# Kernel tuning notes

Hardware: AMD Instinct MI355X
Metric: run time of the kernel (lower is better)

Reference implementation:

```python
import jax, jax.numpy as jnp
import numpy as np

N_SUPPORT = 12800
N_QUERY = 32768
SEQ_LEN = 100
INPUT_DIM = 32
EMBED_DIM = 64
N_CLASSES = 128
EPS = 1e-8


def setup_inputs() -> dict:
    key = jax.random.key(0)
    k1, k2, k3 = jax.random.split(key, 3)
    support = jax.random.normal(k1, (N_SUPPORT, SEQ_LEN, INPUT_DIM), dtype=jnp.float32)
    query = jax.random.normal(k2, (N_QUERY, SEQ_LEN, INPUT_DIM), dtype=jnp.float32)
    # equal shots per class; unique() first-occurrence order == 0..C-1
    support_labels = jnp.arange(N_SUPPORT, dtype=jnp.int64 if jax.config.jax_enable_x64 else jnp.int32) % N_CLASSES
    W = jax.random.normal(k3, (INPUT_DIM, EMBED_DIM), dtype=jnp.float32) * (1.0 / np.sqrt(INPUT_DIM))
    b = jnp.zeros((EMBED_DIM,), dtype=jnp.float32)
    return {"support": support, "support_labels": support_labels, "query": query, "W": W, "b": b}


def _encode(x, W, b):
    # minimal encoder: mean-pool over seq, then linear projection
    return jnp.mean(x, axis=1) @ W + b  # (n, embed_dim)


def reference(support, support_labels, query, W, b):
    se = _encode(support, W, b)   # (n_support, D)
    qe = _encode(query, W, b)     # (n_query, D)
    # per-class mean (segment mean), single fused pass instead of per-class boolean_mask loop
    sums = jax.ops.segment_sum(se, support_labels, num_segments=N_CLASSES)          # (C, D)
    counts = jax.ops.segment_sum(jnp.ones((se.shape[0],), se.dtype), support_labels, num_segments=N_CLASSES)
    prototypes = sums / counts[:, None]                                             # (C, D)
    # pairwise euclidean distance, faithful to expand-subtract-sum formulation
    diff = qe[:, None, :] - prototypes[None, :, :]                                  # (n_query, C, D)
    distances = jnp.sqrt(jnp.sum(diff * diff, axis=2) + EPS)                        # (n_query, C)
    logits = -jnp.square(distances)
    return logits, prototypes
```

## Files before the change

kernel.cpp:

```cpp
#include <hip/hip_runtime.h>

#define SEQ_LEN   100
#define IN_DIM    32
#define EMB       64
#define NCLS      128
#define N_SUPPORT 12800
#define N_QUERY   32768
#define N_ITEMS   (N_SUPPORT + N_QUERY)
#define EPS_F     1e-8f


__global__ __launch_bounds__(256) void zero_ws_k(float* __restrict__ ws, int n) {
    int i = blockIdx.x * 256 + threadIdx.x;
    if (i < n) ws[i] = 0.0f;
}

__global__ __launch_bounds__(256) void encode_all_k(
    const float* __restrict__ support, const int* __restrict__ labels,
    const float* __restrict__ query,   const float* __restrict__ W,
    const float* __restrict__ b,
    float* __restrict__ classSum, float* __restrict__ classCount,
    float* __restrict__ qe)
{
    __shared__ float Wl[IN_DIM * EMB];
    const int t = threadIdx.x;
    #pragma unroll
    for (int j = 0; j < 8; ++j) Wl[t + j * 256] = W[t + j * 256];

    const int lane = t & 63;
    const int wave = t >> 6;
    const int d4 = lane & 7;
    const int ph = lane >> 3;
    const float bd = b[lane];
    __syncthreads();

    const int nWaves = gridDim.x * 4;
    const float s = 1.0f / (float)SEQ_LEN;

    for (int item = blockIdx.x * 4 + wave; item < N_ITEMS; item += nWaves) {
        const bool isSup = item < N_SUPPORT;
        const float* src = isSup
            ? support + (size_t)item * (SEQ_LEN * IN_DIM)
            : query   + (size_t)(item - N_SUPPORT) * (SEQ_LEN * IN_DIM);
        const float4* base = reinterpret_cast<const float4*>(src) + d4;

        float4 acc = make_float4(0.f, 0.f, 0.f, 0.f);
        #pragma unroll
        for (int i = 0; i < 12; ++i) {
            float4 v = base[(ph + 8 * i) * (IN_DIM / 4)];
            acc.x += v.x; acc.y += v.y; acc.z += v.z; acc.w += v.w;
        }
        if (ph < 4) {
            float4 v = base[(ph + 96) * (IN_DIM / 4)];
            acc.x += v.x; acc.y += v.y; acc.z += v.z; acc.w += v.w;
        }
        #pragma unroll
        for (int m = 8; m <= 32; m <<= 1) {
            acc.x += __shfl_xor(acc.x, m);
            acc.y += __shfl_xor(acc.y, m);
            acc.z += __shfl_xor(acc.z, m);
            acc.w += __shfl_xor(acc.w, m);
        }
        acc.x *= s; acc.y *= s; acc.z *= s; acc.w *= s;

        if (isSup) {
            const int lab = labels[item];
            if (lane < 8) {
                float* dst = classSum + lab * IN_DIM + lane * 4;
                atomicAdd(dst + 0, acc.x);
                atomicAdd(dst + 1, acc.y);
                atomicAdd(dst + 2, acc.z);
                atomicAdd(dst + 3, acc.w);
            }
            if (lane == 0) atomicAdd(&classCount[lab], 1.0f);
        } else {
            float a2 = bd;
            #pragma unroll
            for (int k4 = 0; k4 < 8; ++k4) {
                const float px = __shfl(acc.x, k4);
                const float py = __shfl(acc.y, k4);
                const float pz = __shfl(acc.z, k4);
                const float pw = __shfl(acc.w, k4);
                a2 += px * Wl[(k4 * 4 + 0) * EMB + lane];
                a2 += py * Wl[(k4 * 4 + 1) * EMB + lane];
                a2 += pz * Wl[(k4 * 4 + 2) * EMB + lane];
                a2 += pw * Wl[(k4 * 4 + 3) * EMB + lane];
            }
            qe[(size_t)(item - N_SUPPORT) * EMB + lane] = a2;
        }
    }
}

__global__ __launch_bounds__(256) void proto_finalize_k(
    const float* __restrict__ classSum, const float* __restrict__ classCount,
    const float* __restrict__ W, const float* __restrict__ b,
    float* __restrict__ protoOut)
{
    const int idx = blockIdx.x * 256 + threadIdx.x;
    const int c = idx >> 6;
    const int d = idx & 63;
    const float cnt = classCount[c];
    const float inv = (cnt > 0.f) ? (1.0f / cnt) : 0.f;
    float acc = b[d];
    #pragma unroll
    for (int k = 0; k < IN_DIM; ++k)
        acc += classSum[c * IN_DIM + k] * inv * W[k * EMB + d];
    protoOut[idx] = acc;
}

__global__ __launch_bounds__(256) void distances_k(
    const float* __restrict__ qe, const float* __restrict__ proto,
    float* __restrict__ logits)
{
    __shared__ float pl[NCLS * (EMB + 1)];
    __shared__ float ql[16 * EMB];
    const int t = threadIdx.x;
    const int q0 = blockIdx.x * 16;

    #pragma unroll
    for (int j = 0; j < 32; ++j) {
        const int i = t + j * 256;
        pl[(i >> 6) * (EMB + 1) + (i & 63)] = proto[i];
    }
    #pragma unroll
    for (int j = 0; j < 4; ++j) {
        const int i = t + j * 256;
        ql[i] = qe[(size_t)q0 * EMB + i];
    }
    __syncthreads();

    float* outB = logits + (size_t)q0 * NCLS;
    #pragma unroll
    for (int j = 0; j < 8; ++j) {
        const int idx = t + j * 256;
        const int q = idx >> 7;
        const int c = idx & 127;
        const float* qv = ql + q * EMB;
        const float* pv = pl + c * (EMB + 1);
        float s2 = 0.f;
        #pragma unroll
        for (int d = 0; d < EMB; ++d) {
            float df = qv[d] - pv[d];
            s2 += df * df;
        }
        outB[idx] = -(s2 + EPS_F);
    }
}

__device__ inline float4 wave_pool_fb(const float* __restrict__ src, int item, int lane) {
    const int d4 = lane & 7;
    const int ph = lane >> 3;
    const float4* base = reinterpret_cast<const float4*>(src)
                       + (size_t)item * (SEQ_LEN * IN_DIM / 4) + d4;
    float4 acc = make_float4(0.f, 0.f, 0.f, 0.f);
    for (int r = ph; r < SEQ_LEN; r += 8) {
        float4 v = base[r * (IN_DIM / 4)];
        acc.x += v.x; acc.y += v.y; acc.z += v.z; acc.w += v.w;
    }
    #pragma unroll
    for (int m = 8; m <= 32; m <<= 1) {
        acc.x += __shfl_xor(acc.x, m);
        acc.y += __shfl_xor(acc.y, m);
        acc.z += __shfl_xor(acc.z, m);
        acc.w += __shfl_xor(acc.w, m);
    }
    return acc;
}

__global__ __launch_bounds__(256) void support_accum_fb_k(
    const float* __restrict__ support, const int* __restrict__ labels,
    float* __restrict__ classSum, float* __restrict__ classCount)
{
    const int t = threadIdx.x;
    const int wave = t >> 6, lane = t & 63;
    const int item = blockIdx.x * 4 + wave;
    float4 acc = wave_pool_fb(support, item, lane);
    const float s = 1.0f / (float)SEQ_LEN;
    const int lab = labels[item];
    if (lane < 8) {
        float* dst = classSum + lab * IN_DIM + lane * 4;
        atomicAdd(dst + 0, acc.x * s);
        atomicAdd(dst + 1, acc.y * s);
        atomicAdd(dst + 2, acc.z * s);
        atomicAdd(dst + 3, acc.w * s);
    }
    if (lane == 0) atomicAdd(&classCount[lab], 1.0f);
}

__global__ __launch_bounds__(256) void query_logits_fused_k(
    const float* __restrict__ query, const float* __restrict__ W,
    const float* __restrict__ b, const float* __restrict__ proto,
    float* __restrict__ logits)
{
    __shared__ float Wl[IN_DIM * EMB];
    __shared__ float pl[NCLS * (EMB + 1)];
    __shared__ float qel[4 * EMB];
    const int t = threadIdx.x;
    const int wave = t >> 6, lane = t & 63;
    const int q0 = blockIdx.x * 4;

    #pragma unroll
    for (int j = 0; j < 8; ++j) Wl[t + j * 256] = W[t + j * 256];
    #pragma unroll
    for (int j = 0; j < 32; ++j) {
        const int i = t + j * 256;
        pl[(i >> 6) * (EMB + 1) + (i & 63)] = proto[i];
    }
    float4 acc = wave_pool_fb(query, q0 + wave, lane);
    const float s = 1.0f / (float)SEQ_LEN;
    acc.x *= s; acc.y *= s; acc.z *= s; acc.w *= s;
    float a2 = b[lane];
    #pragma unroll
    for (int k4 = 0; k4 < 8; ++k4) {
        const float px = __shfl(acc.x, k4);
        const float py = __shfl(acc.y, k4);
        const float pz = __shfl(acc.z, k4);
        const float pw = __shfl(acc.w, k4);
        a2 += px * Wl[(k4 * 4 + 0) * EMB + lane];
        a2 += py * Wl[(k4 * 4 + 1) * EMB + lane];
        a2 += pz * Wl[(k4 * 4 + 2) * EMB + lane];
        a2 += pw * Wl[(k4 * 4 + 3) * EMB + lane];
    }
    qel[t] = a2;
    __syncthreads();
    float* outB = logits + (size_t)q0 * NCLS;
    #pragma unroll
    for (int j = 0; j < 2; ++j) {
        const int idx = t + j * 256;
        const int q = idx >> 7;
        const int c = idx & 127;
        const float* qv = qel + q * EMB;
        const float* pv = pl + c * (EMB + 1);
        float s2 = 0.f;
        #pragma unroll
        for (int d = 0; d < EMB; ++d) {
            float df = qv[d] - pv[d];
            s2 += df * df;
        }
        outB[idx] = -(s2 + EPS_F);
    }
}

extern "C" void kernel_launch(void* const* d_in, const int* in_sizes, int n_in,
                              void* d_out, int out_size, void* d_ws, size_t ws_size,
                              hipStream_t stream) {
    const float* support = (const float*)d_in[0];
    const int*   labels  = (const int*)d_in[1];
    const float* query   = (const float*)d_in[2];
    const float* W       = (const float*)d_in[3];
    const float* b       = (const float*)d_in[4];

    float* out      = (float*)d_out;
    float* logits   = out;
    float* protoOut = out + (size_t)N_QUERY * NCLS;

    float* classSum   = (float*)d_ws;
    float* classCount = classSum + NCLS * IN_DIM;
    float* qeWs       = classCount + NCLS;
    const int nZero = NCLS * IN_DIM + NCLS;
    const size_t wsNeeded = (size_t)(nZero + N_QUERY * EMB) * sizeof(float);

    zero_ws_k<<<(nZero + 255) / 256, 256, 0, stream>>>(classSum, nZero);

    if (ws_size >= wsNeeded) {
        encode_all_k<<<2048, 256, 0, stream>>>(support, labels, query, W, b,
                                               classSum, classCount, qeWs);
        proto_finalize_k<<<(NCLS * EMB) / 256, 256, 0, stream>>>(classSum, classCount, W, b, protoOut);
        distances_k<<<N_QUERY / 16, 256, 0, stream>>>(qeWs, protoOut, logits);
    } else {
        support_accum_fb_k<<<N_SUPPORT / 4, 256, 0, stream>>>(support, labels, classSum, classCount);
        proto_finalize_k<<<(NCLS * EMB) / 256, 256, 0, stream>>>(classSum, classCount, W, b, protoOut);
        query_logits_fused_k<<<N_QUERY / 4, 256, 0, stream>>>(query, W, b, protoOut, logits);
    }
}
```

Before: 243.6 us.

## Replace grid-stride per-wave encoder with one-block-per-8-items pooling kernel

Swaps the persistent grid-stride encoder, which gave each wave one item, for a non-persistent grid where each block pools 8 items. The four waves split the sequence and combine their partial sums through shared memory. The W load into shared memory now happens only in query blocks, and the projection reads the pooled vectors from shared memory. The aim is more loads in flight per item and less per-item shuffle overhead, at the cost of two block barriers and a much larger grid with per-block W staging.

```diff
diff --git a/kernel.cpp b/kernel.cpp
--- a/kernel.cpp
+++ b/kernel.cpp
@@ -6,8 +6,10 @@
 #define NCLS      128
 #define N_SUPPORT 12800
 #define N_QUERY   32768
-#define N_ITEMS   (N_SUPPORT + N_QUERY)
 #define EPS_F     1e-8f
+
+#define SUP_BLOCKS (N_SUPPORT / 8)
+#define QRY_BLOCKS (N_QUERY / 8)
 
 
 __global__ __launch_bounds__(256) void zero_ws_k(float* __restrict__ ws, int n) {
@@ -15,78 +17,68 @@
     if (i < n) ws[i] = 0.0f;
 }
 
-__global__ __launch_bounds__(256) void encode_all_k(
+__global__ __launch_bounds__(256) void pool_all_k(
     const float* __restrict__ support, const int* __restrict__ labels,
     const float* __restrict__ query,   const float* __restrict__ W,
     const float* __restrict__ b,
     float* __restrict__ classSum, float* __restrict__ classCount,
     float* __restrict__ qe)
 {
-    __shared__ float Wl[IN_DIM * EMB];
-    const int t = threadIdx.x;
-    #pragma unroll
-    for (int j = 0; j < 8; ++j) Wl[t + j * 256] = W[t + j * 256];
-
-    const int lane = t & 63;
-    const int wave = t >> 6;
-    const int d4 = lane & 7;
-    const int ph = lane >> 3;
-    const float bd = b[lane];
-    __syncthreads();
-
-    const int nWaves = gridDim.x * 4;
-    const float s = 1.0f / (float)SEQ_LEN;
-
-    for (int item = blockIdx.x * 4 + wave; item < N_ITEMS; item += nWaves) {
-        const bool isSup = item < N_SUPPORT;
-        const float* src = isSup
-            ? support + (size_t)item * (SEQ_LEN * IN_DIM)
-            : query   + (size_t)(item - N_SUPPORT) * (SEQ_LEN * IN_DIM);
-        const float4* base = reinterpret_cast<const float4*>(src) + d4;
-
-        float4 acc = make_float4(0.f, 0.f, 0.f, 0.f);
-        #pragma unroll
-        for (int i = 0; i < 12; ++i) {
-            float4 v = base[(ph + 8 * i) * (IN_DIM / 4)];
-            acc.x += v.x; acc.y += v.y; acc.z += v.z; acc.w += v.w;
-        }
-        if (ph < 4) {
-            float4 v = base[(ph + 96) * (IN_DIM / 4)];
-            acc.x += v.x; acc.y += v.y; acc.z += v.z; acc.w += v.w;
-        }
-        #pragma unroll
-        for (int m = 8; m <= 32; m <<= 1) {
-            acc.x += __shfl_xor(acc.x, m);
-            acc.y += __shfl_xor(acc.y, m);
-            acc.z += __shfl_xor(acc.z, m);
-            acc.w += __shfl_xor(acc.w, m);
-        }
-        acc.x *= s; acc.y *= s; acc.z *= s; acc.w *= s;
-
-        if (isSup) {
-            const int lab = labels[item];
-            if (lane < 8) {
-                float* dst = classSum + lab * IN_DIM + lane * 4;
-                atomicAdd(dst + 0, acc.x);
-                atomicAdd(dst + 1, acc.y);
-                atomicAdd(dst + 2, acc.z);
-                atomicAdd(dst + 3, acc.w);
-            }
-            if (lane == 0) atomicAdd(&classCount[lab], 1.0f);
-        } else {
-            float a2 = bd;
+    __shared__ float4 red[256];
+    __shared__ float  pooled[8][IN_DIM];
+    __shared__ float  Wl[IN_DIM * EMB];
+    const int t = threadIdx.x;
+    const bool isSup = blockIdx.x < SUP_BLOCKS;
+    const int item0 = (isSup ? blockIdx.x : (blockIdx.x - SUP_BLOCKS)) * 8;
+    const float* src = isSup ? support : query;
+
+    if (!isSup) {
+        #pragma unroll
+        for (int j = 0; j < 8; ++j) Wl[t + j * 256] = W[t + j * 256];
+    }
+
+    const int combo = t & 63;
+    const int li  = combo >> 3;
+    const int d4  = combo & 7;
+    const int rep = t >> 6;
+
+    const float4* base = reinterpret_cast<const float4*>(src)
+                       + (size_t)(item0 + li) * (SEQ_LEN * IN_DIM / 4) + d4;
+    float4 acc = make_float4(0.f, 0.f, 0.f, 0.f);
+    #pragma unroll
+    for (int i = 0; i < 25; ++i) {
+        float4 v = base[(rep + 4 * i) * (IN_DIM / 4)];
+        acc.x += v.x; acc.y += v.y; acc.z += v.z; acc.w += v.w;
+    }
+    red[t] = acc;
+    __syncthreads();
+    if (t < 64) {
+        float4 a = red[t], b2 = red[t + 64], c = red[t + 128], d = red[t + 192];
+        const float s = 1.0f / (float)SEQ_LEN;
+        pooled[li][d4 * 4 + 0] = (a.x + b2.x + c.x + d.x) * s;
+        pooled[li][d4 * 4 + 1] = (a.y + b2.y + c.y + d.y) * s;
+        pooled[li][d4 * 4 + 2] = (a.z + b2.z + c.z + d.z) * s;
+        pooled[li][d4 * 4 + 3] = (a.w + b2.w + c.w + d.w) * s;
+    }
+    __syncthreads();
+
+    if (isSup) {
+        const int li2 = t >> 5;
+        const int k   = t & 31;
+        const int lab = labels[item0 + li2];
+        atomicAdd(&classSum[lab * IN_DIM + k], pooled[li2][k]);
+        if (k == 0) atomicAdd(&classCount[lab], 1.0f);
+    } else {
+        #pragma unroll
+        for (int j = 0; j < 2; ++j) {
+            const int idx = t + j * 256;
+            const int q = idx >> 6;
+            const int d = idx & 63;
+            float a2 = b[d];
             #pragma unroll
-            for (int k4 = 0; k4 < 8; ++k4) {
-                const float px = __shfl(acc.x, k4);
-                const float py = __shfl(acc.y, k4);
-                const float pz = __shfl(acc.z, k4);
-                const float pw = __shfl(acc.w, k4);
-                a2 += px * Wl[(k4 * 4 + 0) * EMB + lane];
-                a2 += py * Wl[(k4 * 4 + 1) * EMB + lane];
-                a2 += pz * Wl[(k4 * 4 + 2) * EMB + lane];
-                a2 += pw * Wl[(k4 * 4 + 3) * EMB + lane];
-            }
-            qe[(size_t)(item - N_SUPPORT) * EMB + lane] = a2;
+            for (int k = 0; k < IN_DIM; ++k)
+                a2 += pooled[q][k] * Wl[k * EMB + d];
+            qe[(size_t)(item0 + q) * EMB + d] = a2;
         }
     }
 }
@@ -263,8 +255,8 @@
     zero_ws_k<<<(nZero + 255) / 256, 256, 0, stream>>>(classSum, nZero);
 
     if (ws_size >= wsNeeded) {
-        encode_all_k<<<2048, 256, 0, stream>>>(support, labels, query, W, b,
-                                               classSum, classCount, qeWs);
+        pool_all_k<<<SUP_BLOCKS + QRY_BLOCKS, 256, 0, stream>>>(
+            support, labels, query, W, b, classSum, classCount, qeWs);
         proto_finalize_k<<<(NCLS * EMB) / 256, 256, 0, stream>>>(classSum, classCount, W, b, protoOut);
         distances_k<<<N_QUERY / 16, 256, 0, stream>>>(qeWs, protoOut, logits);
     } else {
```

Result: faster. 230.0 us (median of 2 runs) (-5.6%).
